# Kernel optimization log

Measured on AMD Instinct MI355X. Metric: run time of the kernel, lower is better.

## Reference

```python
import jax, jax.numpy as jnp
import numpy as np

DIM = 2048
DIM_HEAD = 128
HEADS = 16
FF_INNER = 4 * DIM  # 8192
ATTN_INNER = DIM_HEAD * HEADS  # 2048
FUSED_DIMS = (ATTN_INNER, DIM_HEAD, DIM_HEAD, FF_INNER * 2)
R = 8
B, N = 2, 2048


def setup_inputs() -> dict:
    key = jax.random.key(0)
    ks = jax.random.split(key, 12)
    s = 0.02
    return {
        "x": jax.random.normal(ks[0], (B, N, DIM), jnp.float32),
        "gamma": jnp.ones((DIM,), jnp.float32),
        "w_fused": jax.random.normal(ks[1], (DIM, sum(FUSED_DIMS)), jnp.float32) * s,
        "w_attn_out": jax.random.normal(ks[2], (ATTN_INNER, DIM), jnp.float32) * s,
        "w_ff_out": jax.random.normal(ks[3], (FF_INNER, DIM), jnp.float32) * s,
        "a_q": jax.random.normal(ks[4], (DIM, R), jnp.float32) * s,
        "b_q": jax.random.normal(ks[5], (R, ATTN_INNER), jnp.float32) * s,
        "a_k": jax.random.normal(ks[6], (DIM, R), jnp.float32) * s,
        "b_k": jax.random.normal(ks[7], (R, DIM_HEAD), jnp.float32) * s,
        "a_v": jax.random.normal(ks[8], (DIM, R), jnp.float32) * s,
        "b_v": jax.random.normal(ks[9], (R, DIM_HEAD), jnp.float32) * s,
        "a_o": jax.random.normal(ks[10], (ATTN_INNER, R), jnp.float32) * s,
        "b_o": jax.random.normal(ks[11], (R, DIM), jnp.float32) * s,
    }


def _rotate_half(t):
    t1, t2 = jnp.split(t, 2, axis=-1)
    return jnp.concatenate((-t2, t1), axis=-1)


def _rope(pos, t):
    return t * jnp.cos(pos) + _rotate_half(t) * jnp.sin(pos)


def reference(x, gamma, w_fused, w_attn_out, w_ff_out,
              a_q, b_q, a_k, b_k, a_v, b_v, a_o, b_o):
    b, n, d = x.shape
    # LayerNorm (beta buffer is zeros)
    mu = jnp.mean(x, -1, keepdims=True)
    var = jnp.var(x, -1, keepdims=True)
    xn = (x - mu) * jax.lax.rsqrt(var + 1e-5) * gamma

    proj = xn @ w_fused
    splits = np.cumsum(FUSED_DIMS)[:-1]
    q, k, v, ff = jnp.split(proj, splits, axis=-1)

    # fused QKV LoRA (scale alpha/r = 1)
    q = q + (xn @ a_q) @ b_q
    k = k + (xn @ a_k) @ b_k
    v = v + (xn @ a_v) @ b_v

    q = q.reshape(b, n, HEADS, DIM_HEAD).transpose(0, 2, 1, 3)  # b h n d
    q = q * (DIM_HEAD ** -0.5)

    # rotary embedding
    inv_freq = 1.0 / (10000.0 ** (jnp.arange(0, DIM_HEAD, 2, dtype=jnp.float32) / DIM_HEAD))
    freqs = jnp.arange(n, dtype=jnp.float32)[:, None] * inv_freq[None, :]  # n, d/2
    pos = jnp.concatenate((freqs, freqs), axis=-1)  # n, d
    q = _rope(pos, q)          # broadcast over b,h
    k = _rope(pos, k)          # b n d (single head, MQA)

    sim = jnp.einsum('bhid,bjd->bhij', q, k)
    causal = jnp.triu(jnp.ones((n, n), dtype=bool), 1)
    sim = jnp.where(causal, -jnp.finfo(sim.dtype).max, sim)
    attn = jax.nn.softmax(sim, axis=-1)
    out = jnp.einsum('bhij,bjd->bhid', attn, v)
    out = out.transpose(0, 2, 1, 3).reshape(b, n, ATTN_INNER)

    attn_out = out @ w_attn_out + (out @ a_o) @ b_o

    x1, gate = jnp.split(ff, 2, axis=-1)
    ff_out = (jax.nn.silu(gate) * x1) @ w_ff_out
    return attn_out + ff_out
```

## Files before the change

kernel.cpp:

```cpp
#include <hip/hip_runtime.h>

typedef unsigned short u16;
typedef __attribute__((ext_vector_type(8))) short s8v;
typedef __attribute__((ext_vector_type(4))) float f32x4;

__device__ __forceinline__ u16 f2bf(float f) {
  unsigned int u = __float_as_uint(f);
  u += ((u >> 16) & 1u) + 0x7FFFu;
  return (u16)(u >> 16);
}
__device__ __forceinline__ float bf2f(u16 h) {
  return __uint_as_float(((unsigned int)h) << 16);
}
__device__ __forceinline__ void gl_lds16(const void* g, void* l) {
  __builtin_amdgcn_global_load_lds(
      (__attribute__((address_space(1))) void*)g,
      (__attribute__((address_space(3))) void*)l, 16, 0, 0);
}
__device__ __forceinline__ f32x4 mfma16(s8v a, s8v b, f32x4 c) {
  return __builtin_amdgcn_mfma_f32_16x16x32_bf16(a, b, c, 0, 0, 0);
}

__global__ void transpose_cvt(const float* __restrict__ in, u16* __restrict__ out,
                              int rows, int cols, int ldo) {
  __shared__ float tile[32][33];
  int c0 = blockIdx.x * 32, r0 = blockIdx.y * 32;
  int tx = threadIdx.x, ty = threadIdx.y;
#pragma unroll
  for (int i = 0; i < 4; i++)
    tile[ty + i * 8][tx] = in[(long)(r0 + ty + i * 8) * cols + c0 + tx];
  __syncthreads();
#pragma unroll
  for (int i = 0; i < 4; i++)
    out[(long)(c0 + ty + i * 8) * ldo + r0 + tx] = f2bf(tile[tx][ty + i * 8]);
}

__global__ void vtrans(const u16* __restrict__ proj, u16* __restrict__ v_t) {
  __shared__ u16 tile[32][33];
  int n0 = blockIdx.x * 32, d0 = blockIdx.y * 32, b = blockIdx.z;
  int tx = threadIdx.x, ty = threadIdx.y;
#pragma unroll
  for (int i = 0; i < 4; i++)
    tile[ty + i * 8][tx] =
        proj[((long)b * 2048 + n0 + ty + i * 8) * 18688 + 2176 + d0 + tx];
  __syncthreads();
#pragma unroll
  for (int i = 0; i < 4; i++)
    v_t[((long)b * 128 + d0 + ty + i * 8) * 2048 + n0 + tx] = tile[tx][ty + i * 8];
}

__global__ void fill_aug_k(u16* __restrict__ wt, int N, const float* __restrict__ bq,
                           const float* __restrict__ bk, const float* __restrict__ bv) {
  long idx = (long)blockIdx.x * 256 + threadIdx.x;
  if (idx >= (long)N * 32) return;
  int n = (int)(idx >> 5), j = (int)(idx & 31);
  float v = 0.f;
  if (bq && j < 8 && n < 2048) v = bq[j * 2048 + n];
  else if (bk && j >= 8 && j < 16 && n >= 2048 && n < 2176) v = bk[(j - 8) * 128 + (n - 2048)];
  else if (bv && j >= 16 && j < 24 && n >= 2176 && n < 2304) v = bv[(j - 16) * 128 + (n - 2176)];
  wt[(long)n * 2080 + 2048 + j] = f2bf(v);
}

__global__ __launch_bounds__(256) void layernorm_k(const float* __restrict__ x,
                                                   const float* __restrict__ gamma,
                                                   u16* __restrict__ xn) {
  const int row = blockIdx.x, tid = threadIdx.x;
  const float* xr = x + (long)row * 2048 + tid * 8;
  float4 v0 = *(const float4*)xr;
  float4 v1 = *(const float4*)(xr + 4);
  float vals[8] = {v0.x, v0.y, v0.z, v0.w, v1.x, v1.y, v1.z, v1.w};
  float s = 0.f, q = 0.f;
#pragma unroll
  for (int e = 0; e < 8; e++) { s += vals[e]; q += vals[e] * vals[e]; }
#pragma unroll
  for (int off = 32; off > 0; off >>= 1) {
    s += __shfl_down(s, off, 64);
    q += __shfl_down(q, off, 64);
  }
  __shared__ float red[8];
  const int w = tid >> 6, lane = tid & 63;
  if (lane == 0) { red[w] = s; red[4 + w] = q; }
  __syncthreads();
  if (tid == 0) {
    float S = red[0] + red[1] + red[2] + red[3];
    float Q = red[4] + red[5] + red[6] + red[7];
    float mu = S * (1.f / 2048.f);
    float var = Q * (1.f / 2048.f) - mu * mu;
    red[0] = mu; red[1] = rsqrtf(var + 1e-5f);
  }
  __syncthreads();
  float mu = red[0], rs = red[1];
  const float* g = gamma + tid * 8;
  u16 ov[8];
#pragma unroll
  for (int e = 0; e < 8; e++) ov[e] = f2bf((vals[e] - mu) * rs * g[e]);
  *(s8v*)(xn + (long)row * 2080 + tid * 8) = *(const s8v*)ov;
}

__global__ __launch_bounds__(256) void lora_down_x(u16* __restrict__ xn_aug,
                                                   const float* __restrict__ aq,
                                                   const float* __restrict__ ak,
                                                   const float* __restrict__ av) {
  const int row = blockIdx.x, tid = threadIdx.x;
  s8v xv = *(const s8v*)(xn_aug + (long)row * 2080 + tid * 8);
  float acc[3][8];
#pragma unroll
  for (int m = 0; m < 3; m++)
#pragma unroll
    for (int j = 0; j < 8; j++) acc[m][j] = 0.f;
  const float* mats[3] = {aq, ak, av};
#pragma unroll
  for (int e = 0; e < 8; e++) {
    float xe = bf2f((u16)xv[e]);
    int k = tid * 8 + e;
#pragma unroll
    for (int m = 0; m < 3; m++) {
      const float4* ap = (const float4*)(mats[m] + (long)k * 8);
      float4 a0 = ap[0], a1 = ap[1];
      acc[m][0] += xe * a0.x; acc[m][1] += xe * a0.y;
      acc[m][2] += xe * a0.z; acc[m][3] += xe * a0.w;
      acc[m][4] += xe * a1.x; acc[m][5] += xe * a1.y;
      acc[m][6] += xe * a1.z; acc[m][7] += xe * a1.w;
    }
  }
#pragma unroll
  for (int m = 0; m < 3; m++)
#pragma unroll
    for (int j = 0; j < 8; j++)
#pragma unroll
      for (int off = 32; off > 0; off >>= 1)
        acc[m][j] += __shfl_down(acc[m][j], off, 64);
  __shared__ float red[4][24];
  const int w = tid >> 6, lane = tid & 63;
  if (lane == 0)
    for (int m = 0; m < 3; m++)
      for (int j = 0; j < 8; j++) red[w][m * 8 + j] = acc[m][j];
  __syncthreads();
  if (tid < 32) {
    float v = 0.f;
    if (tid < 24) v = red[0][tid] + red[1][tid] + red[2][tid] + red[3][tid];
    xn_aug[(long)row * 2080 + 2048 + tid] = f2bf(v);
  }
}

__global__ __launch_bounds__(256) void lora_down_ctx(u16* __restrict__ ctx_aug,
                                                     const float* __restrict__ ao) {
  const int row = blockIdx.x, tid = threadIdx.x;
  s8v xv = *(const s8v*)(ctx_aug + (long)row * 2080 + tid * 8);
  float acc[8];
#pragma unroll
  for (int j = 0; j < 8; j++) acc[j] = 0.f;
#pragma unroll
  for (int e = 0; e < 8; e++) {
    float xe = bf2f((u16)xv[e]);
    int k = tid * 8 + e;
    const float4* ap = (const float4*)(ao + (long)k * 8);
    float4 a0 = ap[0], a1 = ap[1];
    acc[0] += xe * a0.x; acc[1] += xe * a0.y; acc[2] += xe * a0.z; acc[3] += xe * a0.w;
    acc[4] += xe * a1.x; acc[5] += xe * a1.y; acc[6] += xe * a1.z; acc[7] += xe * a1.w;
  }
#pragma unroll
  for (int j = 0; j < 8; j++)
#pragma unroll
    for (int off = 32; off > 0; off >>= 1)
      acc[j] += __shfl_down(acc[j], off, 64);
  __shared__ float red[4][8];
  const int w = tid >> 6, lane = tid & 63;
  if (lane == 0)
    for (int j = 0; j < 8; j++) red[w][j] = acc[j];
  __syncthreads();
  if (tid < 32) {
    float v = 0.f;
    if (tid < 8) v = red[0][tid] + red[1][tid] + red[2][tid] + red[3][tid];
    ctx_aug[(long)row * 2080 + 2048 + tid] = f2bf(v);
  }
}

__global__ void rope_k(u16* __restrict__ proj) {
  int idx = blockIdx.x * 256 + threadIdx.x;
  int i = idx & 63;
  int u = (idx >> 6) % 17;
  int row = idx / (17 * 64);
  int n = row & 2047;
  float invf = __powf(10000.f, -(float)i * (1.f / 64.f));
  float ang = (float)n * invf;
  float cs = cosf(ang), sn = sinf(ang);
  int cb = (u < 16) ? u * 128 : 2048;
  u16* p = proj + (long)row * 18688 + cb + i;
  float t1 = bf2f(p[0]), t2 = bf2f(p[64]);
  float sc = (u < 16) ? 0.08838834764831845f : 1.f;
  p[0]  = f2bf((t1 * cs - t2 * sn) * sc);
  p[64] = f2bf((t2 * cs + t1 * sn) * sc);
}

__global__ void silu_mul_k(u16* __restrict__ proj) {
  long idx = (long)blockIdx.x * 256 + threadIdx.x;
  int row = (int)(idx >> 10);
  int c8 = (int)(idx & 1023) * 8;
  u16* px = proj + (long)row * 18688 + 2304 + c8;
  const u16* pg = proj + (long)row * 18688 + 10496 + c8;
  s8v xv = *(const s8v*)px;
  s8v gv = *(const s8v*)pg;
  u16 ov[8];
#pragma unroll
  for (int e = 0; e < 8; e++) {
    float x1 = bf2f((u16)xv[e]);
    float g = bf2f((u16)gv[e]);
    ov[e] = f2bf(x1 * g / (1.f + __expf(-g)));
  }
  *(s8v*)px = *(const s8v*)ov;
}

enum { STORE_BF16 = 0, STORE_F32 = 1, ADD_F32 = 2 };
template <int MODE>
__global__ __launch_bounds__(256, 2) void gemm_bt(const u16* __restrict__ A, int lda,
                                                  const u16* __restrict__ Bt, int ldb,
                                                  void* __restrict__ Cv, int ldc, int K,
                                                  int nbx) {
  const int my = blockIdx.x & 31;
  const int mx = blockIdx.y * 8 + (blockIdx.x >> 5);
  if (mx >= nbx) return;
  __shared__ u16 As[128 * 32];
  __shared__ u16 Bs[128 * 32];
  const int tid = threadIdx.x;
  const int w = tid >> 6, lane = tid & 63, quad = lane >> 4, l15 = lane & 15;
  const int wm = (w >> 1) * 64, wn = (w & 1) * 64;
  const long m0 = (long)my * 128;
  const long n0 = (long)mx * 128;

  const int srow = lane >> 2;
  const int scol = (((lane & 3) ^ ((lane >> 3) & 3)) * 8);
  const int cc0 = w * 2, cc1 = cc0 + 1;
  const u16* ga0 = A + (m0 + cc0 * 16 + srow) * lda + scol;
  const u16* ga1 = A + (m0 + cc1 * 16 + srow) * lda + scol;
  const u16* gb0 = Bt + (n0 + cc0 * 16 + srow) * ldb + scol;
  const u16* gb1 = Bt + (n0 + cc1 * 16 + srow) * ldb + scol;
  u16* la0 = As + cc0 * 512;
  u16* la1 = As + cc1 * 512;
  u16* lb0 = Bs + cc0 * 512;
  u16* lb1 = Bs + cc1 * 512;

  const int sseg = (quad ^ ((l15 >> 1) & 3)) * 8;

  f32x4 acc[4][4];
#pragma unroll
  for (int i = 0; i < 4; i++)
#pragma unroll
    for (int j = 0; j < 4; j++) acc[i][j] = {0.f, 0.f, 0.f, 0.f};

  for (int k0 = 0; k0 < K; k0 += 32) {
    gl_lds16(ga0 + k0, la0);
    gl_lds16(ga1 + k0, la1);
    gl_lds16(gb0 + k0, lb0);
    gl_lds16(gb1 + k0, lb1);
    __syncthreads();
    s8v af[4], bf[4];
#pragma unroll
    for (int mi = 0; mi < 4; mi++)
      af[mi] = *(const s8v*)(As + (wm + mi * 16 + l15) * 32 + sseg);
#pragma unroll
    for (int ni = 0; ni < 4; ni++)
      bf[ni] = *(const s8v*)(Bs + (wn + ni * 16 + l15) * 32 + sseg);
#pragma unroll
    for (int mi = 0; mi < 4; mi++)
#pragma unroll
      for (int ni = 0; ni < 4; ni++)
        acc[mi][ni] = mfma16(af[mi], bf[ni], acc[mi][ni]);
    __syncthreads();
  }
#pragma unroll
  for (int mi = 0; mi < 4; mi++)
#pragma unroll
    for (int r = 0; r < 4; r++) {
      long row = m0 + wm + mi * 16 + quad * 4 + r;
#pragma unroll
      for (int ni = 0; ni < 4; ni++) {
        long col = n0 + wn + ni * 16 + l15;
        float v = acc[mi][ni][r];
        if (MODE == STORE_BF16) ((u16*)Cv)[row * ldc + col] = f2bf(v);
        else if (MODE == STORE_F32) ((float*)Cv)[row * ldc + col] = v;
        else ((float*)Cv)[row * ldc + col] += v;
      }
    }
}

__global__ __launch_bounds__(256) void flash_k(const u16* __restrict__ proj,
                                               const u16* __restrict__ v_t,
                                               u16* __restrict__ ctx) {
  __shared__ u16 Kt[4 * 1024];
  __shared__ u16 Vx[8 * 512];
  __shared__ u16 Pw[4 * 512];
  const int qt = blockIdx.x, h = blockIdx.y, b = blockIdx.z;
  const int tid = threadIdx.x;
  const int w = tid >> 6, lane = tid & 63, quad = lane >> 4, l15 = lane & 15;
  const int qbase = qt * 64 + w * 16;

  s8v qf[4];
  {
    long rowQ = (long)b * 2048 + qbase + l15;
    const u16* qp = proj + rowQ * 18688 + h * 128 + quad * 8;
#pragma unroll
    for (int kk = 0; kk < 4; kk++) qf[kk] = *(const s8v*)(qp + kk * 32);
  }
  f32x4 o[8];
#pragma unroll
  for (int i = 0; i < 8; i++) o[i] = {0.f, 0.f, 0.f, 0.f};
  float m_i[4] = {-1e30f, -1e30f, -1e30f, -1e30f};
  float l_i[4] = {0.f, 0.f, 0.f, 0.f};

  const int srow = lane >> 2;
  const int sseg = ((lane & 3) ^ ((lane >> 3) & 3)) * 8;
  const int rseg = (quad ^ ((l15 >> 1) & 3)) * 8;

  const int nkb = 2 * qt + 2;
  for (int kb = 0; kb < nkb; kb++) {
    const int k0 = kb * 32;
    {
      long rK = (long)b * 2048 + k0;
#pragma unroll
      for (int h2 = 0; h2 < 2; h2++)
        gl_lds16(proj + (rK + h2 * 16 + srow) * 18688 + 2048 + w * 32 + sseg,
                 Kt + w * 1024 + h2 * 512);
#pragma unroll
      for (int h2 = 0; h2 < 2; h2++)
        gl_lds16(v_t + ((long)b * 128 + w * 32 + h2 * 16 + srow) * 2048 + k0 + sseg,
                 Vx + (w * 2 + h2) * 512);
    }
    __syncthreads();
    if (k0 <= qbase + 15) {
      f32x4 s[2];
#pragma unroll
      for (int ni = 0; ni < 2; ni++) {
        f32x4 a = {0.f, 0.f, 0.f, 0.f};
#pragma unroll
        for (int kk = 0; kk < 4; kk++) {
          s8v kf = *(const s8v*)(Kt + kk * 1024 + (ni * 16 + l15) * 32 + rseg);
          a = mfma16(qf[kk], kf, a);
        }
        s[ni] = a;
      }
#pragma unroll
      for (int ni = 0; ni < 2; ni++) {
        int kg = k0 + ni * 16 + l15;
#pragma unroll
        for (int r = 0; r < 4; r++)
          if (kg > qbase + quad * 4 + r) s[ni][r] = -1e30f;
      }
      float al[4];
#pragma unroll
      for (int r = 0; r < 4; r++) {
        float mx = fmaxf(s[0][r], s[1][r]);
#pragma unroll
        for (int off = 8; off > 0; off >>= 1)
          mx = fmaxf(mx, __shfl_xor(mx, off, 16));
        float mn = fmaxf(m_i[r], mx);
        al[r] = __expf(m_i[r] - mn);
        m_i[r] = mn;
      }
#pragma unroll
      for (int ni = 0; ni < 2; ni++)
#pragma unroll
        for (int r = 0; r < 4; r++) s[ni][r] = __expf(s[ni][r] - m_i[r]);
#pragma unroll
      for (int r = 0; r < 4; r++) {
        float rs = s[0][r] + s[1][r];
#pragma unroll
        for (int off = 8; off > 0; off >>= 1)
          rs += __shfl_xor(rs, off, 16);
        l_i[r] = l_i[r] * al[r] + rs;
      }
#pragma unroll
      for (int ni = 0; ni < 2; ni++)
#pragma unroll
        for (int r = 0; r < 4; r++) {
          int p = quad * 4 + r;
          int sg = ni * 2 + (l15 >> 3);
          int sp = sg ^ ((p >> 1) & 3);
          Pw[w * 512 + p * 32 + sp * 8 + (l15 & 7)] = f2bf(s[ni][r]);
        }
      __asm__ volatile("s_waitcnt lgkmcnt(0)" ::: "memory");
#pragma unroll
      for (int nt = 0; nt < 8; nt++)
#pragma unroll
        for (int r = 0; r < 4; r++) o[nt][r] *= al[r];
      s8v pf = *(const s8v*)(Pw + w * 512 + l15 * 32 + rseg);
#pragma unroll
      for (int nt = 0; nt < 8; nt++) {
        s8v vf = *(const s8v*)(Vx + (nt * 16 + l15) * 32 + rseg);
        o[nt] = mfma16(pf, vf, o[nt]);
      }
    }
    __syncthreads();
  }
  float inv[4];
#pragma unroll
  for (int r = 0; r < 4; r++) inv[r] = 1.f / l_i[r];
#pragma unroll
  for (int nt = 0; nt < 8; nt++)
#pragma unroll
    for (int r = 0; r < 4; r++) {
      long row = (long)b * 2048 + qbase + quad * 4 + r;
      ctx[row * 2080 + h * 128 + nt * 16 + l15] = f2bf(o[nt][r] * inv[r]);
    }
}

#define OFF_WF   0L
#define OFF_WO   77742080L
#define OFF_WFF  86261760L
#define OFF_XN   119816192L
#define OFF_PROJ 136855552L
#define OFF_CTX  289947648L
#define WS_NEED  306987008L

extern "C" void kernel_launch(void* const* d_in, const int* in_sizes, int n_in,
                              void* d_out, int out_size, void* d_ws, size_t ws_size,
                              hipStream_t stream) {
  const float* x       = (const float*)d_in[0];
  const float* gamma   = (const float*)d_in[1];
  const float* w_fused = (const float*)d_in[2];
  const float* w_attn  = (const float*)d_in[3];
  const float* w_ff    = (const float*)d_in[4];
  const float* a_q = (const float*)d_in[5];
  const float* b_q = (const float*)d_in[6];
  const float* a_k = (const float*)d_in[7];
  const float* b_k = (const float*)d_in[8];
  const float* a_v = (const float*)d_in[9];
  const float* b_v = (const float*)d_in[10];
  const float* a_o = (const float*)d_in[11];
  const float* b_o = (const float*)d_in[12];
  float* out = (float*)d_out;
  if (ws_size < (size_t)WS_NEED) return;

  char* ws = (char*)d_ws;
  u16* wf_t    = (u16*)(ws + OFF_WF);
  u16* wo_t    = (u16*)(ws + OFF_WO);
  u16* wff_t   = (u16*)(ws + OFF_WFF);
  u16* xn_aug  = (u16*)(ws + OFF_XN);
  u16* v_t     = (u16*)(ws + OFF_XN);
  u16* proj    = (u16*)(ws + OFF_PROJ);
  u16* ctx_aug = (u16*)(ws + OFF_CTX);

  dim3 tb(32, 8);
  transpose_cvt<<<dim3(18688 / 32, 2048 / 32), tb, 0, stream>>>(w_fused, wf_t, 2048, 18688, 2080);
  transpose_cvt<<<dim3(2048 / 32, 2048 / 32), tb, 0, stream>>>(w_attn, wo_t, 2048, 2048, 2080);
  transpose_cvt<<<dim3(2048 / 32, 8192 / 32), tb, 0, stream>>>(w_ff, wff_t, 8192, 2048, 8192);
  fill_aug_k<<<(18688 * 32 + 255) / 256, 256, 0, stream>>>(wf_t, 18688, b_q, b_k, b_v);
  fill_aug_k<<<(2048 * 32 + 255) / 256, 256, 0, stream>>>(wo_t, 2048, b_o, nullptr, nullptr);

  layernorm_k<<<4096, 256, 0, stream>>>(x, gamma, xn_aug);
  lora_down_x<<<4096, 256, 0, stream>>>(xn_aug, a_q, a_k, a_v);

  gemm_bt<STORE_BF16><<<dim3(256, (146 + 7) / 8), 256, 0, stream>>>(
      xn_aug, 2080, wf_t, 2080, proj, 18688, 2080, 146);

  rope_k<<<(4096 * 17 * 64) / 256, 256, 0, stream>>>(proj);
  silu_mul_k<<<(4096 * 1024) / 256, 256, 0, stream>>>(proj);
  vtrans<<<dim3(64, 4, 2), tb, 0, stream>>>(proj, v_t);

  flash_k<<<dim3(32, 16, 2), 256, 0, stream>>>(proj, v_t, ctx_aug);
  lora_down_ctx<<<4096, 256, 0, stream>>>(ctx_aug, a_o);

  gemm_bt<STORE_F32><<<dim3(256, 2), 256, 0, stream>>>(
      ctx_aug, 2080, wo_t, 2080, out, 2048, 2080, 16);
  gemm_bt<ADD_F32><<<dim3(256, 2), 256, 0, stream>>>(
      proj + 2304, 18688, wff_t, 8192, out, 2048, 8192, 16);
}
```

Baseline: 1.452 ms.

## Add 256x256 double-buffered GEMM for fused projection with K padded to 2112

Replaces the generic gemm for the large fused QKV/FF projection with a dedicated 256x256-tile, 512-thread kernel. It uses direct global-to-LDS loads, XOR-swizzled LDS, double buffering with explicit vmcnt waits and barriers, setprio around MFMA, and a grouped block order for L2 locality. The augmented K dimension is padded from 2080 to 2112 so it is a multiple of 64, and the augmentation fill and workspace layout are adjusted to match, with ctx now aliasing the weight buffer. The aim is higher arithmetic intensity and less load stall in the dominant GEMM, at the cost of heavy LDS use (128KB) and more padded K work.

```diff
diff --git a/kernel.cpp b/kernel.cpp
--- a/kernel.cpp
+++ b/kernel.cpp
@@ -49,16 +49,17 @@
     v_t[((long)b * 128 + d0 + ty + i * 8) * 2048 + n0 + tx] = tile[tx][ty + i * 8];
 }
 
-__global__ void fill_aug_k(u16* __restrict__ wt, int N, const float* __restrict__ bq,
-                           const float* __restrict__ bk, const float* __restrict__ bv) {
+__global__ void fill_aug_k(u16* __restrict__ wt, int N, int ldo, int naug,
+                           const float* __restrict__ bq, const float* __restrict__ bk,
+                           const float* __restrict__ bv) {
   long idx = (long)blockIdx.x * 256 + threadIdx.x;
-  if (idx >= (long)N * 32) return;
-  int n = (int)(idx >> 5), j = (int)(idx & 31);
+  if (idx >= (long)N * naug) return;
+  int n = (int)(idx / naug), j = (int)(idx % naug);
   float v = 0.f;
   if (bq && j < 8 && n < 2048) v = bq[j * 2048 + n];
   else if (bk && j >= 8 && j < 16 && n >= 2048 && n < 2176) v = bk[(j - 8) * 128 + (n - 2048)];
   else if (bv && j >= 16 && j < 24 && n >= 2176 && n < 2304) v = bv[(j - 16) * 128 + (n - 2176)];
-  wt[(long)n * 2080 + 2048 + j] = f2bf(v);
+  wt[(long)n * ldo + 2048 + j] = f2bf(v);
 }
 
 __global__ __launch_bounds__(256) void layernorm_k(const float* __restrict__ x,
@@ -94,7 +95,7 @@
   u16 ov[8];
 #pragma unroll
   for (int e = 0; e < 8; e++) ov[e] = f2bf((vals[e] - mu) * rs * g[e]);
-  *(s8v*)(xn + (long)row * 2080 + tid * 8) = *(const s8v*)ov;
+  *(s8v*)(xn + (long)row * 2112 + tid * 8) = *(const s8v*)ov;
 }
 
 __global__ __launch_bounds__(256) void lora_down_x(u16* __restrict__ xn_aug,
@@ -102,7 +103,7 @@
                                                    const float* __restrict__ ak,
                                                    const float* __restrict__ av) {
   const int row = blockIdx.x, tid = threadIdx.x;
-  s8v xv = *(const s8v*)(xn_aug + (long)row * 2080 + tid * 8);
+  s8v xv = *(const s8v*)(xn_aug + (long)row * 2112 + tid * 8);
   float acc[3][8];
 #pragma unroll
   for (int m = 0; m < 3; m++)
@@ -136,10 +137,10 @@
     for (int m = 0; m < 3; m++)
       for (int j = 0; j < 8; j++) red[w][m * 8 + j] = acc[m][j];
   __syncthreads();
-  if (tid < 32) {
+  if (tid < 64) {
     float v = 0.f;
     if (tid < 24) v = red[0][tid] + red[1][tid] + red[2][tid] + red[3][tid];
-    xn_aug[(long)row * 2080 + 2048 + tid] = f2bf(v);
+    xn_aug[(long)row * 2112 + 2048 + tid] = f2bf(v);
   }
 }
 
@@ -284,6 +285,115 @@
     }
 }
 
+__global__ __launch_bounds__(512, 2) void gemm256_bt(const u16* __restrict__ A,
+                                                     const u16* __restrict__ Bt,
+                                                     u16* __restrict__ C, int K) {
+  __shared__ u16 sh[65536];
+  const int cpx = gridDim.x >> 3;
+  const int swz = (blockIdx.x & 7) * cpx + (blockIdx.x >> 3);
+  const int bm = swz & 15;
+  const int bn = swz >> 4;
+  const int tid = threadIdx.x;
+  const int w = tid >> 6, lane = tid & 63;
+  const int quad = lane >> 4, l15 = lane & 15;
+  const int wm = w >> 2, wn = w & 3;
+  const int rseg = (quad ^ ((l15 >> 1) & 3)) * 8;
+  const int aoff = (wm * 128 + l15) * 32 + rseg;
+  const int boff = (wn * 64 + l15) * 32 + rseg;
+  const int srow = lane >> 2;
+  const int sseg = ((lane & 3) ^ ((lane >> 3) & 3)) * 8;
+  const u16* aSrc = A + (long)(bm * 256 + w * 16 + srow) * 2112 + sseg;
+  const u16* bSrc = Bt + (long)(bn * 256 + w * 16 + srow) * 2112 + sseg;
+  u16* stW = sh + w * 512;
+  const int NT = K >> 6;
+
+  f32x4 acc[8][4];
+#pragma unroll
+  for (int i = 0; i < 8; i++)
+#pragma unroll
+    for (int j = 0; j < 4; j++) acc[i][j] = {0.f, 0.f, 0.f, 0.f};
+
+  gl_lds16(aSrc, stW);
+  gl_lds16(bSrc, stW + 16384);
+  gl_lds16(aSrc + 128L * 2112, stW + 4096);
+  gl_lds16(bSrc + 128L * 2112, stW + 16384 + 4096);
+  gl_lds16(aSrc + 32, stW + 8192);
+  gl_lds16(bSrc + 32, stW + 16384 + 8192);
+  gl_lds16(aSrc + 128L * 2112 + 32, stW + 8192 + 4096);
+  gl_lds16(bSrc + 128L * 2112 + 32, stW + 16384 + 8192 + 4096);
+  asm volatile("s_waitcnt vmcnt(4)" ::: "memory");
+  __builtin_amdgcn_s_barrier();
+
+  s8v bf[4];
+  int kcol = 64;
+
+#define STAGE_UNIT(CUR, KK, MH)                                               \
+  gl_lds16(aSrc + (MH) * (128L * 2112) + kcol + (KK) * 32,                    \
+           stW + (((CUR) ^ 1) * 32768) + (KK) * 8192 + (MH) * 4096);          \
+  gl_lds16(bSrc + (MH) * (128L * 2112) + kcol + (KK) * 32,                    \
+           stW + (((CUR) ^ 1) * 32768) + 16384 + (KK) * 8192 + (MH) * 4096);
+
+#define PHASE(CUR, KK, MH, DOB, STG, VM)                                      \
+  {                                                                           \
+    const u16* Ab = sh + (CUR) * 32768 + (KK) * 8192 + aoff + (MH) * 2048;    \
+    s8v af0 = *(const s8v*)(Ab);                                              \
+    s8v af1 = *(const s8v*)(Ab + 512);                                        \
+    s8v af2 = *(const s8v*)(Ab + 1024);                                       \
+    s8v af3 = *(const s8v*)(Ab + 1536);                                       \
+    if (DOB) {                                                                \
+      const u16* Bb = sh + (CUR) * 32768 + 16384 + (KK) * 8192 + boff;        \
+      bf[0] = *(const s8v*)(Bb);                                              \
+      bf[1] = *(const s8v*)(Bb + 512);                                        \
+      bf[2] = *(const s8v*)(Bb + 1024);                                       \
+      bf[3] = *(const s8v*)(Bb + 1536);                                       \
+    }                                                                         \
+    if (STG) { STAGE_UNIT(CUR, KK, MH) }                                      \
+    __builtin_amdgcn_s_barrier();                                             \
+    __builtin_amdgcn_s_setprio(1);                                            \
+    _Pragma("unroll") for (int ni = 0; ni < 4; ni++) {                        \
+      acc[(MH) * 4 + 0][ni] = mfma16(af0, bf[ni], acc[(MH) * 4 + 0][ni]);     \
+      acc[(MH) * 4 + 1][ni] = mfma16(af1, bf[ni], acc[(MH) * 4 + 1][ni]);     \
+      acc[(MH) * 4 + 2][ni] = mfma16(af2, bf[ni], acc[(MH) * 4 + 2][ni]);     \
+      acc[(MH) * 4 + 3][ni] = mfma16(af3, bf[ni], acc[(MH) * 4 + 3][ni]);     \
+    }                                                                         \
+    __builtin_amdgcn_s_setprio(0);                                            \
+    if ((VM) == 4) asm volatile("s_waitcnt vmcnt(4)" ::: "memory");           \
+    if ((VM) == 0) asm volatile("s_waitcnt vmcnt(0)" ::: "memory");           \
+    __builtin_amdgcn_s_barrier();                                             \
+  }
+
+#define TILE(CUR, STG, VM1, VM3)   \
+  PHASE(CUR, 0, 0, 1, STG, -1)     \
+  PHASE(CUR, 0, 1, 0, STG, VM1)    \
+  PHASE(CUR, 1, 0, 1, STG, -1)     \
+  PHASE(CUR, 1, 1, 0, STG, VM3)    \
+  kcol += 64;
+
+  for (int t2 = 0; t2 < NT - 1; t2 += 2) {
+    TILE(0, 1, 4, 4)
+    TILE(1, 1, 4, 4)
+  }
+  TILE(0, 0, 0, -1)
+
+#undef TILE
+#undef PHASE
+#undef STAGE_UNIT
+
+  const long m0 = (long)bm * 256 + wm * 128;
+  const long n0 = (long)bn * 256 + wn * 64;
+#pragma unroll
+  for (int mi = 0; mi < 8; mi++)
+#pragma unroll
+    for (int r = 0; r < 4; r++) {
+      long row = m0 + mi * 16 + quad * 4 + r;
+#pragma unroll
+      for (int ni = 0; ni < 4; ni++) {
+        long col = n0 + ni * 16 + l15;
+        C[row * 18688 + col] = f2bf(acc[mi][ni][r]);
+      }
+    }
+}
+
 __global__ __launch_bounds__(256) void flash_k(const u16* __restrict__ proj,
                                                const u16* __restrict__ v_t,
                                                u16* __restrict__ ctx) {
@@ -405,12 +515,11 @@
 }
 
 #define OFF_WF   0L
-#define OFF_WO   77742080L
-#define OFF_WFF  86261760L
-#define OFF_XN   119816192L
-#define OFF_PROJ 136855552L
-#define OFF_CTX  289947648L
-#define WS_NEED  306987008L
+#define OFF_WO   78938112L
+#define OFF_WFF  87457792L
+#define OFF_XN   121012224L
+#define OFF_PROJ 138313728L
+#define WS_NEED  291405824L
 
 extern "C" void kernel_launch(void* const* d_in, const int* in_sizes, int n_in,
                               void* d_out, int out_size, void* d_ws, size_t ws_size,
@@ -433,25 +542,24 @@
 
   char* ws = (char*)d_ws;
   u16* wf_t    = (u16*)(ws + OFF_WF);
+  u16* ctx_aug = (u16*)(ws + OFF_WF);
   u16* wo_t    = (u16*)(ws + OFF_WO);
   u16* wff_t   = (u16*)(ws + OFF_WFF);
   u16* xn_aug  = (u16*)(ws + OFF_XN);
   u16* v_t     = (u16*)(ws + OFF_XN);
   u16* proj    = (u16*)(ws + OFF_PROJ);
-  u16* ctx_aug = (u16*)(ws + OFF_CTX);
 
   dim3 tb(32, 8);
-  transpose_cvt<<<dim3(18688 / 32, 2048 / 32), tb, 0, stream>>>(w_fused, wf_t, 2048, 18688, 2080);
+  transpose_cvt<<<dim3(18688 / 32, 2048 / 32), tb, 0, stream>>>(w_fused, wf_t, 2048, 18688, 2112);
   transpose_cvt<<<dim3(2048 / 32, 2048 / 32), tb, 0, stream>>>(w_attn, wo_t, 2048, 2048, 2080);
   transpose_cvt<<<dim3(2048 / 32, 8192 / 32), tb, 0, stream>>>(w_ff, wff_t, 8192, 2048, 8192);
-  fill_aug_k<<<(18688 * 32 + 255) / 256, 256, 0, stream>>>(wf_t, 18688, b_q, b_k, b_v);
-  fill_aug_k<<<(2048 * 32 + 255) / 256, 256, 0, stream>>>(wo_t, 2048, b_o, nullptr, nullptr);
+  fill_aug_k<<<(18688 * 64 + 255) / 256, 256, 0, stream>>>(wf_t, 18688, 2112, 64, b_q, b_k, b_v);
+  fill_aug_k<<<(2048 * 32 + 255) / 256, 256, 0, stream>>>(wo_t, 2048, 2080, 32, b_o, nullptr, nullptr);
 
   layernorm_k<<<4096, 256, 0, stream>>>(x, gamma, xn_aug);
   lora_down_x<<<4096, 256, 0, stream>>>(xn_aug, a_q, a_k, a_v);
 
-  gemm_bt<STORE_BF16><<<dim3(256, (146 + 7) / 8), 256, 0, stream>>>(
-      xn_aug, 2080, wf_t, 2080, proj, 18688, 2080, 146);
+  gemm256_bt<<<dim3(16 * (18688 / 256)), 512, 0, stream>>>(xn_aug, wf_t, proj, 2112);
 
   rope_k<<<(4096 * 17 * 64) / 256, 256, 0, stream>>>(proj);
   silu_mul_k<<<(4096 * 1024) / 256, 256, 0, stream>>>(proj);
```

Result: faster. 1.383 ms (-4.8%).
